# Performance work log

Measured on AMD Instinct MI355X. Metric: run time of the kernel, lower is better.

Reference implementation:

```python
import jax, jax.numpy as jnp
import numpy as np

S, N, F, H, O = 64, 4096, 32, 64, 2  # seq_len, n_nodes, nfeat, nhid, nout


def setup_inputs() -> dict:
    key = jax.random.key(0)
    ks = jax.random.split(key, 8)
    sc = 0.02
    return {
        "x": jax.random.normal(ks[0], (S, N, F), jnp.float32),
        "adj": jax.random.uniform(ks[1], (N, N), jnp.float32) / N,  # dense normalized-ish adjacency
        "W1": jax.random.normal(ks[2], (F, H), jnp.float32) * sc,
        "b1": jnp.zeros((H,), jnp.float32),
        "W2": jax.random.normal(ks[3], (H, O), jnp.float32) * sc,
        "b2": jnp.zeros((O,), jnp.float32),
        "Wih0": jax.random.normal(ks[4], (3 * H, O * N), jnp.float32) * sc,
        "Whh0": jax.random.normal(ks[5], (3 * H, H), jnp.float32) * sc,
        "bih0": jnp.zeros((3 * H,), jnp.float32),
        "bhh0": jnp.zeros((3 * H,), jnp.float32),
        "Wih1": jax.random.normal(ks[6], (3 * H, H), jnp.float32) * sc,
        "Whh1": jax.random.normal(ks[7], (3 * H, H), jnp.float32) * sc,
        "bih1": jnp.zeros((3 * H,), jnp.float32),
        "bhh1": jnp.zeros((3 * H,), jnp.float32),
    }


def _gru_layer(xs, Wih, Whh, bih, bhh):
    # xs: (S, B, in); PyTorch GRU cell semantics, h0 = 0
    B = xs.shape[1]
    h0 = jnp.zeros((B, Whh.shape[1]), xs.dtype)

    def step(h, x_t):
        gi = x_t @ Wih.T + bih            # (B, 3H)
        gh = h @ Whh.T + bhh              # (B, 3H)
        ir, iz, inn = jnp.split(gi, 3, axis=-1)
        hr, hz, hn = jnp.split(gh, 3, axis=-1)
        r = jax.nn.sigmoid(ir + hr)
        z = jax.nn.sigmoid(iz + hz)
        n = jnp.tanh(inn + r * hn)
        h_new = (1.0 - z) * n + z * h
        return h_new, h_new

    hT, ys = jax.lax.scan(step, h0, xs)
    return ys, hT


def reference(x, adj, W1, b1, W2, b2, Wih0, Whh0, bih0, bhh0, Wih1, Whh1, bih1, bhh1):
    # GCN per timestep (vectorized over time): adj @ (x @ W) + b, relu, adj @ (. @ W2) + b2, log_softmax
    # dropout inactive (eval mode)
    support = jnp.einsum('snf,fh->snh', x, W1) + b1          # (S, N, H)
    h = jnp.einsum('ij,sjh->sih', adj, support)              # (S, N, H)
    h = jax.nn.relu(h)
    support2 = jnp.einsum('snh,ho->sno', h, W2) + b2         # (S, N, O)
    g = jnp.einsum('ij,sjo->sio', adj, support2)             # (S, N, O)
    logp = jax.nn.log_softmax(g, axis=-1)                    # dim=1 of (N, O) per node
    rnn_in = logp.reshape(S, 1, N * O)                       # batch = 1 (torch.stack construction)
    ys0, h0T = _gru_layer(rnn_in, Wih0, Whh0, bih0, bhh0)
    ys1, h1T = _gru_layer(ys0, Wih1, Whh1, bih1, bhh1)
    hn = jnp.stack([h0T, h1T])                               # (n_layers, 1, H)
    return ys1, hn
```

## Files before the change

kernel.cpp:

```cpp
#include <hip/hip_runtime.h>
#include <stdint.h>

#define SS 64
#define NN 4096
#define FF 32
#define HH 64
#define OO 2
#define G3 192

typedef float f32x4 __attribute__((ext_vector_type(4)));
typedef short bf16x8 __attribute__((ext_vector_type(8)));
typedef unsigned short u16x8 __attribute__((ext_vector_type(8)));
typedef long longx2 __attribute__((ext_vector_type(2)));

#define AS1 __attribute__((address_space(1)))
#define AS3 __attribute__((address_space(3)))

__device__ __forceinline__ unsigned short f2bf(float f) {
  union { float f; uint32_t u; } v; v.f = f;
  uint32_t u = v.u;
  uint32_t r = (u + 0x7FFFu + ((u >> 16) & 1u)) >> 16;
  return (unsigned short)r;
}
__device__ __forceinline__ float bf2f(unsigned short s) {
  union { uint32_t u; float f; } v; v.u = ((uint32_t)s) << 16;
  return v.f;
}
__device__ __forceinline__ unsigned char f2e4m3(float x) {
  float a = fabsf(x);
  unsigned s = (x < 0.f) ? 0x80u : 0u;
  if (a >= 448.f) return (unsigned char)(s | 0x7E);
  if (a < 0.015625f) {
    int q = (int)rintf(a * 512.f);
    return (unsigned char)(s | (unsigned)q);
  }
  union { float f; uint32_t u; } v; v.f = a;
  uint32_t b = v.u + 0x7FFFFu + ((v.u >> 20) & 1u);
  int e = (int)(b >> 23) - 127;
  if (e > 8) return (unsigned char)(s | 0x7E);
  return (unsigned char)(s | (unsigned)(((e + 7) << 3) | ((b >> 20) & 7u)));
}
__device__ __forceinline__ int kperm128(int i) {
  int b = (i >> 3) & 15;
  int np = ((b & 7) << 1) | (b >> 3);
  return (i & ~127) | (np << 3) | (i & 7);
}

__global__ __launch_bounds__(256) void k_prep(const float* __restrict__ adj,
                                              unsigned char* __restrict__ adj8,
                                              float* __restrict__ rowsum,
                                              const float* __restrict__ x,
                                              unsigned char* __restrict__ Xt8) {
  __shared__ float xl[64][33];
  __shared__ float ps[4];
  int tid = threadIdx.x;
  if (blockIdx.x < 4096) {
    int row = blockIdx.x;
    const float4* src = (const float4*)(adj + (size_t)row * 4096);
    uchar4* dst8 = (uchar4*)(adj8 + (size_t)row * 4096);
    float sum = 0.f;
    #pragma unroll
    for (int q = 0; q < 4; ++q) {
      int idx = q * 256 + tid;
      float4 v = src[idx];
      uchar4 r8;
      r8.x = f2e4m3(v.x * 4096.f); r8.y = f2e4m3(v.y * 4096.f);
      r8.z = f2e4m3(v.z * 4096.f); r8.w = f2e4m3(v.w * 4096.f);
      int b = (idx >> 1) & 15;
      int np = ((b & 7) << 1) | (b >> 3);
      int nidx = (idx & ~31) | (np << 1) | (idx & 1);
      dst8[nidx] = r8;
      sum += (v.x + v.y) + (v.z + v.w);
    }
    #pragma unroll
    for (int off = 1; off < 64; off <<= 1) sum += __shfl_xor(sum, off);
    if ((tid & 63) == 0) ps[tid >> 6] = sum;
    __syncthreads();
    if (tid == 0) rowsum[row] = (ps[0] + ps[1]) + (ps[2] + ps[3]);
    return;
  }
  int bs = blockIdx.x - 4096;
  int s = bs >> 6, jb = (bs & 63) << 6;
  const float4* xg = (const float4*)(x + ((size_t)s * NN + jb) * FF);
  #pragma unroll
  for (int ii = 0; ii < 2; ++ii) {
    int idx = tid + ii * 256;
    float4 v = xg[idx];
    int j = idx >> 3, f = (idx & 7) << 2;
    xl[j][f] = v.x; xl[j][f + 1] = v.y; xl[j][f + 2] = v.z; xl[j][f + 3] = v.w;
  }
  __syncthreads();
  int f = tid >> 3, jc = tid & 7;
  unsigned int lo = 0, hi = 0;
  #pragma unroll
  for (int jj = 0; jj < 4; ++jj) lo |= ((unsigned int)f2e4m3(xl[jc * 8 + jj][f])) << (jj * 8);
  #pragma unroll
  for (int jj = 0; jj < 4; ++jj) hi |= ((unsigned int)f2e4m3(xl[jc * 8 + 4 + jj][f])) << (jj * 8);
  uint2 ov; ov.x = lo; ov.y = hi;
  int np = (jc << 1) | ((jb >> 6) & 1);
  *(uint2*)(Xt8 + (size_t)(s * 32 + f) * 4096 + (jb & ~127) + np * 8) = ov;
}

#define SBAR()   asm volatile("s_barrier" ::: "memory")
#define VMC8()   asm volatile("s_waitcnt vmcnt(8)" ::: "memory")
#define VMC6()   asm volatile("s_waitcnt vmcnt(6)" ::: "memory")
#define VMC0()   asm volatile("s_waitcnt vmcnt(0)" ::: "memory")

__global__ __launch_bounds__(512, 2) void k_gemmAX(
    const unsigned char* __restrict__ A8,
    const unsigned char* __restrict__ B8,
    const float* __restrict__ rowsum,
    const float* __restrict__ W1f,
    const float* __restrict__ b1f,
    const float* __restrict__ W2f,
    const float* __restrict__ b2f,
    unsigned char* __restrict__ B2t8) {
  __shared__ __align__(16) char lds[147456];
  __shared__ __align__(16) unsigned short w1t[64 * 40];
  __shared__ float w2l[128];
  __shared__ float b1l[64];
  __shared__ float b2l[2];
  const int tid = threadIdx.x;
  const int wid = tid >> 6, l = tid & 63;
  const int wr2 = wid >> 2, wc2 = wid & 3;
  const int lc = l & 15, lq = l >> 4;

  {
    float4 v = ((const float4*)W1f)[tid];
    int f = tid >> 4, h = (tid & 15) * 4;
    w1t[(h + 0) * 40 + f] = f2bf(v.x);
    w1t[(h + 1) * 40 + f] = f2bf(v.y);
    w1t[(h + 2) * 40 + f] = f2bf(v.z);
    w1t[(h + 3) * 40 + f] = f2bf(v.w);
  }
  if (tid < 32) *(float4*)&w2l[tid * 4] = ((const float4*)W2f)[tid];
  if (tid < 16) *(float4*)&b1l[tid * 4] = ((const float4*)b1f)[tid];
  if (tid < 2) b2l[tid] = b2f[tid];
  __syncthreads();

  int bid = blockIdx.x;
  int swz = (bid & 7) * 32 + (bid >> 3);
  const int i0 = (swz >> 3) * 128;
  const int c0 = (swz & 7) * 256;

  const int aBase = (wr2 * 64 + lc) * 128;
  const int bBase = 16384 + (wc2 * 64 + lc) * 128;
  const int cLo = ((lq ^ (lc & 7)) << 4);
  const int cHi = (((4 + lq) ^ (lc & 7)) << 4);

  const int srow = wid * 8 + (l >> 3);
  const int scol = (((l & 7) ^ (srow & 7)) << 4);
  const char* gA = (const char*)A8 + (size_t)(i0 + srow) * 4096 + scol;
  const char* gB = (const char*)B8 + (size_t)(c0 + srow) * 4096 + scol;
  char* ldsW = (char*)lds + wid * 1024;
  const char* ldsR = (const char*)lds;

  f32x4 acc[4][4];
  #pragma unroll
  for (int m = 0; m < 4; ++m)
    #pragma unroll
    for (int n = 0; n < 4; ++n) acc[m][n] = {0.f, 0.f, 0.f, 0.f};

  longx2 afq[4], bfq[4];

#define STAGE6(KT, BOFS) do {                                                        \
    __builtin_amdgcn_global_load_lds((const AS1 void*)(gA + (KT) * 128),             \
        (AS3 void*)(ldsW + (BOFS)), 16, 0, 0);                                       \
    __builtin_amdgcn_global_load_lds((const AS1 void*)(gA + 262144 + (KT) * 128),    \
        (AS3 void*)(ldsW + (BOFS) + 8192), 16, 0, 0);                                \
    __builtin_amdgcn_global_load_lds((const AS1 void*)(gB + (KT) * 128),             \
        (AS3 void*)(ldsW + (BOFS) + 16384), 16, 0, 0);                               \
    __builtin_amdgcn_global_load_lds((const AS1 void*)(gB + 262144 + (KT) * 128),    \
        (AS3 void*)(ldsW + (BOFS) + 24576), 16, 0, 0);                               \
    __builtin_amdgcn_global_load_lds((const AS1 void*)(gB + 524288 + (KT) * 128),    \
        (AS3 void*)(ldsW + (BOFS) + 32768), 16, 0, 0);                               \
    __builtin_amdgcn_global_load_lds((const AS1 void*)(gB + 786432 + (KT) * 128),    \
        (AS3 void*)(ldsW + (BOFS) + 40960), 16, 0, 0);                               \
  } while (0)

#define READ_CH(BOFS, CK) do {                                                       \
    _Pragma("unroll")                                                                \
    for (int _m = 0; _m < 4; ++_m)                                                   \
      afq[_m] = *(const longx2*)(ldsR + (BOFS) + aBase + _m * 2048 + (CK));          \
    _Pragma("unroll")                                                                \
    for (int _n = 0; _n < 4; ++_n)                                                   \
      bfq[_n] = *(const longx2*)(ldsR + (BOFS) + bBase + _n * 2048 + (CK));          \
  } while (0)

#define MFMA2K() do {                                                                \
    __builtin_amdgcn_s_setprio(1);                                                   \
    _Pragma("unroll")                                                                \
    for (int _kk = 0; _kk < 2; ++_kk)                                                \
      _Pragma("unroll")                                                              \
      for (int _m = 0; _m < 4; ++_m)                                                 \
        _Pragma("unroll")                                                            \
        for (int _n = 0; _n < 4; ++_n)                                               \
          acc[_m][_n] = __builtin_amdgcn_mfma_f32_16x16x32_fp8_fp8(                  \
              afq[_m][_kk], bfq[_n][_kk], acc[_m][_n], 0, 0, 0);                     \
    __builtin_amdgcn_s_setprio(0);                                                   \
  } while (0)

  STAGE6(0, 0);
  STAGE6(1, 49152);
  VMC6();
  SBAR();

  int bR = 0, bS = 98304;
  for (int kt = 0; kt < 30; ++kt) {
    READ_CH(bR, cLo);
    STAGE6(kt + 2, bS);
    MFMA2K();
    READ_CH(bR, cHi);
    MFMA2K();
    VMC6();
    SBAR();
    bR = (bR == 98304) ? 0 : bR + 49152;
    bS = (bS == 98304) ? 0 : bS + 49152;
  }
  READ_CH(bR, cLo); MFMA2K(); READ_CH(bR, cHi); MFMA2K();
  VMC0(); SBAR(); bR = (bR == 98304) ? 0 : bR + 49152;
  READ_CH(bR, cLo); MFMA2K(); READ_CH(bR, cHi); MFMA2K();
  __syncthreads();

  unsigned short* C1L = (unsigned short*)lds;
  {
    const int rb = wr2 * 64 + lq * 4;
    const int cbL = wc2 * 64 + lc;
    #pragma unroll
    for (int m = 0; m < 4; ++m)
      #pragma unroll
      for (int r = 0; r < 4; ++r) {
        const int row = rb + m * 16 + r;
        #pragma unroll
        for (int n = 0; n < 4; ++n)
          C1L[row * 264 + cbL + n * 16] = f2bf(acc[m][n][r] * 0.000244140625f);
      }
  }
  __syncthreads();

  {
    const f32x4 zacc = {0.f, 0.f, 0.f, 0.f};
    bf16x8 bw[4];
    float b1v[4], w2a[4], w2b[4];
    #pragma unroll
    for (int n = 0; n < 4; ++n) {
      const int h = n * 16 + lc;
      bw[n] = *(const bf16x8*)((const char*)w1t + h * 80 + lq * 16);
      b1v[n] = b1l[h];
      w2a[n] = w2l[h * 2];
      w2b[n] = w2l[h * 2 + 1];
    }
    const int rbase = wid * 16 + lq * 4;
    const float4 rs4 = *(const float4*)&rowsum[i0 + rbase];
    const float bo0 = b2l[0], bo1 = b2l[1];
    #pragma unroll
    for (int s = 0; s < 8; ++s) {
      bf16x8 afe = *(const bf16x8*)((const char*)C1L +
                     (wid * 16 + lc) * 528 + s * 64 + lq * 16);
      float o0r[4] = {0.f, 0.f, 0.f, 0.f};
      float o1r[4] = {0.f, 0.f, 0.f, 0.f};
      #pragma unroll
      for (int n = 0; n < 4; ++n) {
        f32x4 hq = __builtin_amdgcn_mfma_f32_16x16x32_bf16(afe, bw[n], zacc, 0, 0, 0);
        #pragma unroll
        for (int r = 0; r < 4; ++r) {
          float hv = hq[r] + rs4[r] * b1v[n];
          hv = hv > 0.f ? hv : 0.f;
          o0r[r] += hv * w2a[n];
          o1r[r] += hv * w2b[n];
        }
      }
      #pragma unroll
      for (int off = 1; off < 16; off <<= 1)
        #pragma unroll
        for (int r = 0; r < 4; ++r) {
          o0r[r] += __shfl_xor(o0r[r], off);
          o1r[r] += __shfl_xor(o1r[r], off);
        }
      if (lc == 0) {
        const int sg = (c0 >> 5) + s;
        #pragma unroll
        for (int r = 0; r < 4; ++r) {
          const int ip = kperm128(i0 + rbase + r);
          B2t8[(size_t)(sg * 2 + 0) * 4096 + ip] = f2e4m3((o0r[r] + bo0) * 4096.f);
          B2t8[(size_t)(sg * 2 + 1) * 4096 + ip] = f2e4m3((o1r[r] + bo1) * 4096.f);
        }
      }
    }
  }
}

__global__ __launch_bounds__(256) void k_gemm2f8(
    const unsigned char* __restrict__ A8,
    const unsigned char* __restrict__ B8,
    float* __restrict__ Gp) {
  __shared__ __align__(16) char lds[98304];
  const int tid = threadIdx.x;
  const int wid = tid >> 6, l = tid & 63;
  const int wr = wid >> 1, wc = wid & 1;
  const int lc = l & 15, lq = l >> 4;
  const int bi = blockIdx.x & 31, ks = blockIdx.x >> 5;
  const int i0 = bi * 128;
  const size_t kbase = (size_t)ks * 512;

  const int aBase = (wr * 64 + lc) * 128;
  const int bBase = 16384 + (wc * 64 + lc) * 128;
  const int cLo = ((lq ^ (lc & 7)) << 4);
  const int cHi = (((4 + lq) ^ (lc & 7)) << 4);

  const int srow = wid * 8 + (l >> 3);
  const int scol = (((l & 7) ^ (srow & 7)) << 4);
  const char* gA = (const char*)A8 + (size_t)(i0 + srow) * 4096 + kbase + scol;
  const char* gB = (const char*)B8 + (size_t)srow * 4096 + kbase + scol;
  char* ldsW = (char*)lds + wid * 1024;
  const char* ldsR = (const char*)lds;

  f32x4 acc[4][4];
  #pragma unroll
  for (int m = 0; m < 4; ++m)
    #pragma unroll
    for (int n = 0; n < 4; ++n) acc[m][n] = {0.f, 0.f, 0.f, 0.f};

  longx2 afq[4], bfq[4];

#define G2STAGE(KT, BOFS) do {                                                       \
    __builtin_amdgcn_global_load_lds((const AS1 void*)(gA + (KT) * 128),             \
        (AS3 void*)(ldsW + (BOFS)), 16, 0, 0);                                       \
    __builtin_amdgcn_global_load_lds((const AS1 void*)(gA + 131072 + (KT) * 128),    \
        (AS3 void*)(ldsW + (BOFS) + 4096), 16, 0, 0);                                \
    __builtin_amdgcn_global_load_lds((const AS1 void*)(gA + 262144 + (KT) * 128),    \
        (AS3 void*)(ldsW + (BOFS) + 8192), 16, 0, 0);                                \
    __builtin_amdgcn_global_load_lds((const AS1 void*)(gA + 393216 + (KT) * 128),    \
        (AS3 void*)(ldsW + (BOFS) + 12288), 16, 0, 0);                               \
    __builtin_amdgcn_global_load_lds((const AS1 void*)(gB + (KT) * 128),             \
        (AS3 void*)(ldsW + (BOFS) + 16384), 16, 0, 0);                               \
    __builtin_amdgcn_global_load_lds((const AS1 void*)(gB + 131072 + (KT) * 128),    \
        (AS3 void*)(ldsW + (BOFS) + 20480), 16, 0, 0);                               \
    __builtin_amdgcn_global_load_lds((const AS1 void*)(gB + 262144 + (KT) * 128),    \
        (AS3 void*)(ldsW + (BOFS) + 24576), 16, 0, 0);                               \
    __builtin_amdgcn_global_load_lds((const AS1 void*)(gB + 393216 + (KT) * 128),    \
        (AS3 void*)(ldsW + (BOFS) + 28672), 16, 0, 0);                               \
  } while (0)

#define G2READ(BOFS, CK) do {                                                        \
    _Pragma("unroll")                                                                \
    for (int _m = 0; _m < 4; ++_m)                                                   \
      afq[_m] = *(const longx2*)(ldsR + (BOFS) + aBase + _m * 2048 + (CK));          \
    _Pragma("unroll")                                                                \
    for (int _n = 0; _n < 4; ++_n)                                                   \
      bfq[_n] = *(const longx2*)(ldsR + (BOFS) + bBase + _n * 2048 + (CK));          \
  } while (0)

#define G2MFMA() do {                                                                \
    __builtin_amdgcn_s_setprio(1);                                                   \
    _Pragma("unroll")                                                                \
    for (int _kk = 0; _kk < 2; ++_kk)                                                \
      _Pragma("unroll")                                                              \
      for (int _m = 0; _m < 4; ++_m)                                                 \
        _Pragma("unroll")                                                            \
        for (int _n = 0; _n < 4; ++_n)                                               \
          acc[_m][_n] = __builtin_amdgcn_mfma_f32_16x16x32_fp8_fp8(                  \
              afq[_m][_kk], bfq[_n][_kk], acc[_m][_n], 0, 0, 0);                     \
    __builtin_amdgcn_s_setprio(0);                                                   \
  } while (0)

  G2STAGE(0, 0);
  G2STAGE(1, 32768);
  VMC8();
  SBAR();

  G2READ(0, cLo); G2STAGE(2, 65536); G2MFMA(); G2READ(0, cHi); G2MFMA();
  VMC8(); SBAR();
  G2READ(32768, cLo); G2STAGE(3, 0); G2MFMA(); G2READ(32768, cHi); G2MFMA();
  VMC8(); SBAR();
  G2READ(65536, cLo); G2MFMA(); G2READ(65536, cHi); G2MFMA();
  VMC0(); SBAR();
  G2READ(0, cLo); G2MFMA(); G2READ(0, cHi); G2MFMA();

  float* outp = Gp + (size_t)ks * 524288;
  const int rbase = i0 + wr * 64 + lq * 4;
  const int cbase = wc * 64 + lc;
  #pragma unroll
  for (int m = 0; m < 4; ++m)
    #pragma unroll
    for (int n = 0; n < 4; ++n)
      #pragma unroll
      for (int r = 0; r < 4; ++r)
        outp[(size_t)(rbase + m * 16 + r) * 128 + cbase + n * 16] =
            acc[m][n][r] * 5.9604644775390625e-8f;
}

__global__ __launch_bounds__(256) void k_lsm(const float* __restrict__ Gp,
                                             float* __restrict__ Rm) {
  __shared__ float Gacc[32][130];
  int i0 = blockIdx.x * 32;
  int tid = threadIdx.x;
  float4 v[4];
  #pragma unroll
  for (int i = 0; i < 4; ++i) v[i] = {0.f, 0.f, 0.f, 0.f};
  for (int ks = 0; ks < 8; ++ks) {
    const float4* gp4 = ((const float4*)Gp) + (size_t)ks * 131072 + (size_t)i0 * 32;
    #pragma unroll
    for (int i = 0; i < 4; ++i) {
      float4 t = gp4[tid + i * 256];
      v[i].x += t.x; v[i].y += t.y; v[i].z += t.z; v[i].w += t.w;
    }
  }
  #pragma unroll
  for (int i = 0; i < 4; ++i) {
    int f4i = tid + i * 256, row = f4i >> 5, c = (f4i & 31) * 4;
    Gacc[row][c] = v[i].x; Gacc[row][c + 1] = v[i].y;
    Gacc[row][c + 2] = v[i].z; Gacc[row][c + 3] = v[i].w;
  }
  __syncthreads();
  #pragma unroll
  for (int j = 0; j < 8; ++j) {
    int p = j * 256 + tid;
    int ii = p & 31, s = p >> 5;
    float g0 = Gacc[ii][s * 2], g1 = Gacc[ii][s * 2 + 1];
    float m = fmaxf(g0, g1);
    float lse = m + logf(expf(g0 - m) + expf(g1 - m));
    float2 o_; o_.x = g0 - lse; o_.y = g1 - lse;
    *((float2*)(Rm + (size_t)s * 8192 + (size_t)(i0 + ii) * 2)) = o_;
  }
}

__global__ __launch_bounds__(256) void k_gi0(const float* __restrict__ Rm,
                                             const float* __restrict__ Wih0,
                                             float* __restrict__ part) {
  __shared__ float4 Wl[4 * 128];
  int gb = blockIdx.x % 48, ks = blockIdx.x / 48;
  int c0 = ks * 512;
  int tid = threadIdx.x;
  #pragma unroll
  for (int i = 0; i < 2; ++i) {
    int idx = tid + i * 256;
    int g = idx >> 7, c4 = idx & 127;
    Wl[g * 128 + c4] = ((const float4*)(Wih0 + (size_t)(gb * 4 + g) * 8192 + c0))[c4];
  }
  __syncthreads();
  int w = tid >> 6, lane = tid & 63;
  for (int pass = 0; pass < 16; ++pass) {
    int t = pass * 4 + w;
    float a0 = 0.f, a1 = 0.f, a2 = 0.f, a3 = 0.f;
    const float4* rg = (const float4*)(Rm + (size_t)t * 8192 + c0);
    #pragma unroll
    for (int i = 0; i < 2; ++i) {
      int c4 = i * 64 + lane;
      float4 r4 = rg[c4];
      float4 w0 = Wl[c4], w1 = Wl[128 + c4], w2 = Wl[256 + c4], w3 = Wl[384 + c4];
      a0 += r4.x * w0.x + r4.y * w0.y + r4.z * w0.z + r4.w * w0.w;
      a1 += r4.x * w1.x + r4.y * w1.y + r4.z * w1.z + r4.w * w1.w;
      a2 += r4.x * w2.x + r4.y * w2.y + r4.z * w2.z + r4.w * w2.w;
      a3 += r4.x * w3.x + r4.y * w3.y + r4.z * w3.z + r4.w * w3.w;
    }
    #pragma unroll
    for (int off = 1; off < 64; off <<= 1) {
      a0 += __shfl_xor(a0, off);
      a1 += __shfl_xor(a1, off);
      a2 += __shfl_xor(a2, off);
      a3 += __shfl_xor(a3, off);
    }
    if (lane == 0) {
      float4 o_; o_.x = a0; o_.y = a1; o_.z = a2; o_.w = a3;
      *((float4*)(part + ((size_t)ks * 64 + t) * 192 + gb * 4)) = o_;
    }
  }
}

__global__ __launch_bounds__(256) void k_gi0red(const float* __restrict__ part,
                                                const float* __restrict__ bih0,
                                                float* __restrict__ gi0) {
  int idx = blockIdx.x * 256 + threadIdx.x;
  if (idx < 12288) {
    float s_ = bih0[idx % 192];
    for (int ks = 0; ks < 16; ++ks) s_ += part[ks * 12288 + idx];
    gi0[idx] = s_;
  }
}

__device__ __forceinline__ float fsigm(float x) {
  return __builtin_amdgcn_rcpf(1.f + __expf(-x));
}
__device__ __forceinline__ float ftanh(float x) {
  return 1.f - 2.f * __builtin_amdgcn_rcpf(1.f + __expf(2.f * x));
}

__global__ __launch_bounds__(384) void k_gru(const float* __restrict__ gi0,
                                             const float* __restrict__ Whh0,
                                             const float* __restrict__ bhh0,
                                             const float* __restrict__ Wih1,
                                             const float* __restrict__ Whh1,
                                             const float* __restrict__ bih1,
                                             const float* __restrict__ bhh1,
                                             float* __restrict__ out) {
  __shared__ float gil[64][192];
  __shared__ float gout[576];
  __shared__ __align__(16) unsigned short hv[2][64];
  const int tid = threadIdx.x;
  const int w = tid >> 6, l = tid & 63;
  const int matw = w >> 1, half = w & 1;
  const float* Wm = (matw == 0) ? Whh0 : (matw == 1 ? Wih1 : Whh1);
  const int mi = (matw == 2) ? 1 : 0;

  bf16x8 afr[6][2];
  #pragma unroll
  for (int rbi = 0; rbi < 6; ++rbi) {
    int g = (half * 6 + rbi) * 16 + (l & 15);
    #pragma unroll
    for (int kh = 0; kh < 2; ++kh) {
      int k0 = kh * 32 + (l >> 4) * 8;
      const float4* src = (const float4*)(Wm + (size_t)g * 64 + k0);
      float4 v0 = src[0], v1 = src[1];
      bf16x8 a;
      a[0] = (short)f2bf(v0.x); a[1] = (short)f2bf(v0.y);
      a[2] = (short)f2bf(v0.z); a[3] = (short)f2bf(v0.w);
      a[4] = (short)f2bf(v1.x); a[5] = (short)f2bf(v1.y);
      a[6] = (short)f2bf(v1.z); a[7] = (short)f2bf(v1.w);
      afr[rbi][kh] = a;
    }
  }
  {
    float4* gf = (float4*)&gil[0][0];
    const float4* gs = (const float4*)gi0;
    #pragma unroll
    for (int i = 0; i < 8; ++i) gf[i * 384 + tid] = gs[i * 384 + tid];
  }
  if (tid < 128) hv[tid >> 6][tid & 63] = 0;

  float hreg = 0.f;
  float bR = 0.f, bZ = 0.f, bNa = 0.f, bNb = 0.f;
  if (tid < 64) {
    bR = bhh0[tid]; bZ = bhh0[64 + tid]; bNa = bhh0[128 + tid];
  } else if (tid < 128) {
    int g = tid - 64;
    bR = bih1[g] + bhh1[g];
    bZ = bih1[64 + g] + bhh1[64 + g];
    bNa = bih1[128 + g];
    bNb = bhh1[128 + g];
  }
  asm volatile("s_waitcnt lgkmcnt(0)\n\ts_barrier" ::: "memory");

  const int gwb = matw * 192 + half * 96 + (l >> 4) * 4;
  const f32x4 zacc = {0.f, 0.f, 0.f, 0.f};

  for (int i = 0; i <= 64; ++i) {
    bf16x8 b0 = *(const bf16x8*)&hv[mi][(l >> 4) * 8];
    bf16x8 b1 = *(const bf16x8*)&hv[mi][32 + (l >> 4) * 8];
    #pragma unroll
    for (int rbi = 0; rbi < 6; ++rbi) {
      f32x4 a_ = __builtin_amdgcn_mfma_f32_16x16x32_bf16(afr[rbi][0], b0, zacc, 0, 0, 0);
      a_ = __builtin_amdgcn_mfma_f32_16x16x32_bf16(afr[rbi][1], b1, a_, 0, 0, 0);
      if (!(l & 15)) *(f32x4*)&gout[gwb + rbi * 16] = a_;
    }
    asm volatile("s_waitcnt lgkmcnt(0)\n\ts_barrier" ::: "memory");
    if (tid < 64) {
      if (i < 64) {
        float r = fsigm(gil[i][tid] + gout[tid] + bR);
        float z = fsigm(gil[i][64 + tid] + gout[64 + tid] + bZ);
        float n = ftanh(gil[i][128 + tid] + r * (gout[128 + tid] + bNa));
        hreg = (1.f - z) * n + z * hreg;
        hv[0][tid] = f2bf(hreg);
      }
    } else if (tid < 128 && i > 0) {
      int g = tid - 64;
      float r = fsigm(gout[192 + g] + gout[384 + g] + bR);
      float z = fsigm(gout[256 + g] + gout[448 + g] + bZ);
      float n = ftanh((gout[320 + g] + bNa) + r * (gout[512 + g] + bNb));
      hreg = (1.f - z) * n + z * hreg;
      hv[1][g] = f2bf(hreg);
      out[(i - 1) * 64 + g] = hreg;
    }
    asm volatile("s_waitcnt lgkmcnt(0)\n\ts_barrier" ::: "memory");
  }
  if (tid < 64) out[4096 + tid] = hreg;
  else if (tid < 128) out[4096 + 64 + (tid - 64)] = hreg;
}

extern "C" void kernel_launch(void* const* d_in, const int* in_sizes, int n_in,
                              void* d_out, int out_size, void* d_ws, size_t ws_size,
                              hipStream_t stream) {
  const float* x    = (const float*)d_in[0];
  const float* adj  = (const float*)d_in[1];
  const float* W1   = (const float*)d_in[2];
  const float* b1   = (const float*)d_in[3];
  const float* W2   = (const float*)d_in[4];
  const float* b2   = (const float*)d_in[5];
  const float* Wih0 = (const float*)d_in[6];
  const float* Whh0 = (const float*)d_in[7];
  const float* bih0 = (const float*)d_in[8];
  const float* bhh0 = (const float*)d_in[9];
  const float* Wih1 = (const float*)d_in[10];
  const float* Whh1 = (const float*)d_in[11];
  const float* bih1 = (const float*)d_in[12];
  const float* bhh1 = (const float*)d_in[13];
  float* out = (float*)d_out;

  char* ws = (char*)d_ws;
  unsigned char* adj8  = (unsigned char*)ws;
  unsigned char* Xt8   = (unsigned char*)(ws + 16777216);
  float* rowsum        = (float*)(ws + 25165824);
  float* Gp            = (float*)(ws + 25182208);
  float* Rm            = (float*)(ws + 41959424);
  float* part          = (float*)(ws + 44056576);
  float* gi0           = (float*)(ws + 44843008);
  unsigned char* B2t8  = (unsigned char*)(ws + 44892160);

  k_prep<<<8192, 256, 0, stream>>>(adj, adj8, rowsum, x, Xt8);
  k_gemmAX<<<256, 512, 0, stream>>>(adj8, Xt8, rowsum, W1, b1, W2, b2, B2t8);
  k_gemm2f8<<<256, 256, 0, stream>>>(adj8, B2t8, Gp);
  k_lsm<<<128, 256, 0, stream>>>(Gp, Rm);
  k_gi0<<<768, 256, 0, stream>>>(Rm, Wih0, part);
  k_gi0red<<<48, 256, 0, stream>>>(part, bih0, gi0);
  k_gru<<<1, 384, 0, stream>>>(gi0, Whh0, bhh0, Wih1, Whh1, bih1, bhh1, out);
}
```

Baseline: 148.9 us.

## Drop GRU second barrier via per-wave redundant gates and fold gi0 reduction into atomics

The GRU recurrence now double-buffers the gate-product scratch by step parity. Every wave computes the gate update for the layer it needs and keeps its own copy of the hidden state, so each step needs one workgroup barrier instead of two. Separately, the k_gi0red reduction kernel is removed. k_lsm seeds gi0 with the bias and k_gi0 accumulates its partial dot products with float atomicAdd. This saves a launch and a pass over the partials, but the summation order becomes nondeterministic and adds atomic contention.

```diff
diff --git a/kernel.cpp b/kernel.cpp
--- a/kernel.cpp
+++ b/kernel.cpp
@@ -391,7 +391,9 @@
 }
 
 __global__ __launch_bounds__(256) void k_lsm(const float* __restrict__ Gp,
-                                             float* __restrict__ Rm) {
+                                             float* __restrict__ Rm,
+                                             const float* __restrict__ bih0,
+                                             float* __restrict__ gi0) {
   __shared__ float Gacc[32][130];
   int i0 = blockIdx.x * 32;
   int tid = threadIdx.x;
@@ -423,11 +425,18 @@
     float2 o_; o_.x = g0 - lse; o_.y = g1 - lse;
     *((float2*)(Rm + (size_t)s * 8192 + (size_t)(i0 + ii) * 2)) = o_;
   }
+  {
+    int base = blockIdx.x * 96;
+    if (tid < 96) {
+      int idx = base + tid;
+      gi0[idx] = bih0[idx % 192];
+    }
+  }
 }
 
 __global__ __launch_bounds__(256) void k_gi0(const float* __restrict__ Rm,
                                              const float* __restrict__ Wih0,
-                                             float* __restrict__ part) {
+                                             float* __restrict__ gi0) {
   __shared__ float4 Wl[4 * 128];
   int gb = blockIdx.x % 48, ks = blockIdx.x / 48;
   int c0 = ks * 512;
@@ -462,20 +471,12 @@
       a3 += __shfl_xor(a3, off);
     }
     if (lane == 0) {
-      float4 o_; o_.x = a0; o_.y = a1; o_.z = a2; o_.w = a3;
-      *((float4*)(part + ((size_t)ks * 64 + t) * 192 + gb * 4)) = o_;
-    }
-  }
-}
-
-__global__ __launch_bounds__(256) void k_gi0red(const float* __restrict__ part,
-                                                const float* __restrict__ bih0,
-                                                float* __restrict__ gi0) {
-  int idx = blockIdx.x * 256 + threadIdx.x;
-  if (idx < 12288) {
-    float s_ = bih0[idx % 192];
-    for (int ks = 0; ks < 16; ++ks) s_ += part[ks * 12288 + idx];
-    gi0[idx] = s_;
+      float* dst = gi0 + (size_t)t * 192 + gb * 4;
+      atomicAdd(dst + 0, a0);
+      atomicAdd(dst + 1, a1);
+      atomicAdd(dst + 2, a2);
+      atomicAdd(dst + 3, a3);
+    }
   }
 }
 
@@ -495,8 +496,8 @@
                                              const float* __restrict__ bhh1,
                                              float* __restrict__ out) {
   __shared__ float gil[64][192];
-  __shared__ float gout[576];
-  __shared__ __align__(16) unsigned short hv[2][64];
+  __shared__ float gout[2][576];
+  __shared__ __align__(16) unsigned short hvp[6][64];
   const int tid = threadIdx.x;
   const int w = tid >> 6, l = tid & 63;
   const int matw = w >> 1, half = w & 1;
@@ -526,18 +527,17 @@
     #pragma unroll
     for (int i = 0; i < 8; ++i) gf[i * 384 + tid] = gs[i * 384 + tid];
   }
-  if (tid < 128) hv[tid >> 6][tid & 63] = 0;
+  hvp[w][l] = 0;
 
   float hreg = 0.f;
-  float bR = 0.f, bZ = 0.f, bNa = 0.f, bNb = 0.f;
-  if (tid < 64) {
-    bR = bhh0[tid]; bZ = bhh0[64 + tid]; bNa = bhh0[128 + tid];
-  } else if (tid < 128) {
-    int g = tid - 64;
-    bR = bih1[g] + bhh1[g];
-    bZ = bih1[64 + g] + bhh1[64 + g];
-    bNa = bih1[128 + g];
-    bNb = bhh1[128 + g];
+  float bR, bZ, bNa, bNb = 0.f;
+  if (mi == 0) {
+    bR = bhh0[l]; bZ = bhh0[64 + l]; bNa = bhh0[128 + l];
+  } else {
+    bR = bih1[l] + bhh1[l];
+    bZ = bih1[64 + l] + bhh1[64 + l];
+    bNa = bih1[128 + l];
+    bNb = bhh1[128 + l];
   }
   asm volatile("s_waitcnt lgkmcnt(0)\n\ts_barrier" ::: "memory");
 
@@ -545,36 +545,42 @@
   const f32x4 zacc = {0.f, 0.f, 0.f, 0.f};
 
   for (int i = 0; i <= 64; ++i) {
-    bf16x8 b0 = *(const bf16x8*)&hv[mi][(l >> 4) * 8];
-    bf16x8 b1 = *(const bf16x8*)&hv[mi][32 + (l >> 4) * 8];
+    const int par = i & 1;
+    bf16x8 b0 = *(const bf16x8*)&hvp[w][(l >> 4) * 8];
+    bf16x8 b1 = *(const bf16x8*)&hvp[w][32 + (l >> 4) * 8];
     #pragma unroll
     for (int rbi = 0; rbi < 6; ++rbi) {
       f32x4 a_ = __builtin_amdgcn_mfma_f32_16x16x32_bf16(afr[rbi][0], b0, zacc, 0, 0, 0);
       a_ = __builtin_amdgcn_mfma_f32_16x16x32_bf16(afr[rbi][1], b1, a_, 0, 0, 0);
-      if (!(l & 15)) *(f32x4*)&gout[gwb + rbi * 16] = a_;
+      if (!(l & 15)) *(f32x4*)&gout[par][gwb + rbi * 16] = a_;
     }
     asm volatile("s_waitcnt lgkmcnt(0)\n\ts_barrier" ::: "memory");
-    if (tid < 64) {
+    if (mi == 0) {
       if (i < 64) {
-        float r = fsigm(gil[i][tid] + gout[tid] + bR);
-        float z = fsigm(gil[i][64 + tid] + gout[64 + tid] + bZ);
-        float n = ftanh(gil[i][128 + tid] + r * (gout[128 + tid] + bNa));
+        float g0 = gout[par][l], g1 = gout[par][64 + l], g2 = gout[par][128 + l];
+        float r = fsigm(gil[i][l] + g0 + bR);
+        float z = fsigm(gil[i][64 + l] + g1 + bZ);
+        float n = ftanh(gil[i][128 + l] + r * (g2 + bNa));
         hreg = (1.f - z) * n + z * hreg;
-        hv[0][tid] = f2bf(hreg);
+        hvp[w][l] = f2bf(hreg);
       }
-    } else if (tid < 128 && i > 0) {
-      int g = tid - 64;
-      float r = fsigm(gout[192 + g] + gout[384 + g] + bR);
-      float z = fsigm(gout[256 + g] + gout[448 + g] + bZ);
-      float n = ftanh((gout[320 + g] + bNa) + r * (gout[512 + g] + bNb));
-      hreg = (1.f - z) * n + z * hreg;
-      hv[1][g] = f2bf(hreg);
-      out[(i - 1) * 64 + g] = hreg;
-    }
-    asm volatile("s_waitcnt lgkmcnt(0)\n\ts_barrier" ::: "memory");
-  }
-  if (tid < 64) out[4096 + tid] = hreg;
-  else if (tid < 128) out[4096 + 64 + (tid - 64)] = hreg;
+    } else {
+      if (i > 0) {
+        float u0 = gout[par][192 + l], u1 = gout[par][256 + l], u2 = gout[par][320 + l];
+        float v0 = gout[par][384 + l], v1 = gout[par][448 + l], v2 = gout[par][512 + l];
+        float r = fsigm(u0 + v0 + bR);
+        float z = fsigm(u1 + v1 + bZ);
+        float n = ftanh((u2 + bNa) + r * (v2 + bNb));
+        hreg = (1.f - z) * n + z * hreg;
+        hvp[w][l] = f2bf(hreg);
+        if (half == 0) out[(i - 1) * 64 + l] = hreg;
+      }
+    }
+    asm volatile("s_waitcnt lgkmcnt(0)" ::: "memory");
+    __builtin_amdgcn_sched_barrier(0);
+  }
+  if (w == 0) out[4096 + l] = hreg;
+  if (w == 4) out[4096 + 64 + l] = hreg;
 }
 
 extern "C" void kernel_launch(void* const* d_in, const int* in_sizes, int n_in,
@@ -602,15 +608,13 @@
   float* rowsum        = (float*)(ws + 25165824);
   float* Gp            = (float*)(ws + 25182208);
   float* Rm            = (float*)(ws + 41959424);
-  float* part          = (float*)(ws + 44056576);
-  float* gi0           = (float*)(ws + 44843008);
-  unsigned char* B2t8  = (unsigned char*)(ws + 44892160);
+  float* gi0           = (float*)(ws + 44056576);
+  unsigned char* B2t8  = (unsigned char*)(ws + 44105728);
 
   k_prep<<<8192, 256, 0, stream>>>(adj, adj8, rowsum, x, Xt8);
   k_gemmAX<<<256, 512, 0, stream>>>(adj8, Xt8, rowsum, W1, b1, W2, b2, B2t8);
   k_gemm2f8<<<256, 256, 0, stream>>>(adj8, B2t8, Gp);
-  k_lsm<<<128, 256, 0, stream>>>(Gp, Rm);
-  k_gi0<<<768, 256, 0, stream>>>(Rm, Wih0, part);
-  k_gi0red<<<48, 256, 0, stream>>>(part, bih0, gi0);
+  k_lsm<<<128, 256, 0, stream>>>(Gp, Rm, bih0, gi0);
+  k_gi0<<<768, 256, 0, stream>>>(Rm, Wih0, gi0);
   k_gru<<<1, 384, 0, stream>>>(gi0, Whh0, bhh0, Wih1, Whh1, bih1, bhh1, out);
 }
```

Result: slower. 162.1 us (+8.9%).
